# Performance work log

Measured on AMD Instinct MI355X. Metric: run time of the kernel, lower is better.

Reference implementation:

```python
import jax, jax.numpy as jnp
import numpy as np

HIDDEN = 2880
N_HEADS = 64
N_KV_HEADS = 8
HEAD_DIM = 64
ROPE_THETA = 150000.0


def _rope(x, position_ids):
    # x: [B, H, S, D]; rotate-half RoPE as in the flax module
    inv_freq = 1.0 / (ROPE_THETA ** (jnp.arange(0, HEAD_DIM, 2, dtype=jnp.float32) / HEAD_DIM))
    b, h, s, d = x.shape
    freqs = jnp.outer(position_ids.reshape(-1).astype(jnp.float32), inv_freq)  # [B*S, D/2]
    cos = jnp.cos(freqs).reshape(b, 1, s, d // 2)
    sin = jnp.sin(freqs).reshape(b, 1, s, d // 2)
    x1, x2 = jnp.split(x, 2, axis=-1)
    return jnp.concatenate([x1 * cos - x2 * sin, x1 * sin + x2 * cos], axis=-1)


def setup_inputs() -> dict:
    key = jax.random.key(0)
    ks = jax.random.split(key, 5)
    B, S = 2, 1024
    x = jax.random.normal(ks[0], (B, S, HIDDEN), dtype=jnp.float32)
    wq = jax.random.normal(ks[1], (HIDDEN, N_HEADS * HEAD_DIM), dtype=jnp.float32) * 0.02
    wk = jax.random.normal(ks[2], (HIDDEN, N_KV_HEADS * HEAD_DIM), dtype=jnp.float32) * 0.02
    wv = jax.random.normal(ks[3], (HIDDEN, N_KV_HEADS * HEAD_DIM), dtype=jnp.float32) * 0.02
    wo = jax.random.normal(ks[4], (N_HEADS * HEAD_DIM, HIDDEN), dtype=jnp.float32) * 0.02
    position_ids = jnp.broadcast_to(jnp.arange(S, dtype=jnp.int32)[None, :], (B, S))
    return {"x": x, "wq": wq, "wk": wk, "wv": wv, "wo": wo, "position_ids": position_ids}


def reference(x, wq, wk, wv, wo, position_ids):
    b, s, _ = x.shape
    scale = 1.0 / np.sqrt(HEAD_DIM)
    q = (x @ wq).reshape(b, s, N_HEADS, HEAD_DIM).transpose(0, 2, 1, 3)       # [B,H,S,D]
    k = (x @ wk).reshape(b, s, N_KV_HEADS, HEAD_DIM).transpose(0, 2, 1, 3)    # [B,Hkv,S,D]
    v = (x @ wv).reshape(b, s, N_KV_HEADS, HEAD_DIM).transpose(0, 2, 1, 3)
    q = _rope(q, position_ids)
    k = _rope(k, position_ids)
    rep = N_HEADS // N_KV_HEADS
    k = jnp.repeat(k, rep, axis=1)  # GQA head-repeat as in original
    v = jnp.repeat(v, rep, axis=1)
    scores = jnp.einsum('bhqd,bhkd->bhqk', q, k) * scale
    causal = jnp.tril(jnp.ones((s, s), dtype=bool))[None, None, :, :]
    scores = jnp.where(causal, scores, -jnp.inf)
    probs = jax.nn.softmax(scores, axis=-1)
    out = jnp.einsum('bhqk,bhkd->bhqd', probs, v)
    out = out.transpose(0, 2, 1, 3).reshape(b, s, N_HEADS * HEAD_DIM)
    return out @ wo
```

## Files before the change

### kernel.cpp

```cpp
#include <hip/hip_runtime.h>

#define BB 2
#define SS 1024
#define HIDDEN 2880
#define NH 64
#define NKV 8
#define HD 64
#define M_TOK 2048
#define NQ 4096
#define NKVD 512
#define NQKV 5120
#define NOUT 2880
#define NOUT_PAD 2944

typedef __attribute__((ext_vector_type(8))) short short8;
typedef __attribute__((ext_vector_type(4))) float f32x4;

__device__ __forceinline__ unsigned short f2b(float x) {
  union { float f; unsigned u; } v; v.f = x;
  unsigned r = (v.u + 0x7FFFu + ((v.u >> 16) & 1u)) >> 16;
  return (unsigned short)r;
}

__device__ __forceinline__ void gload16(const void* g, void* l) {
  __builtin_amdgcn_global_load_lds(
      (const __attribute__((address_space(1))) void*)g,
      (__attribute__((address_space(3))) void*)l, 16, 0, 0);
}

__global__ __launch_bounds__(256) void cast_x_kernel(const float* __restrict__ in,
                                                     unsigned short* __restrict__ out,
                                                     int n4) {
  int idx = blockIdx.x * 256 + threadIdx.x;
  if (idx >= n4) return;
  float4 v = ((const float4*)in)[idx];
  ushort4 o;
  o.x = f2b(v.x); o.y = f2b(v.y); o.z = f2b(v.z); o.w = f2b(v.w);
  ((ushort4*)out)[idx] = o;
}

__global__ __launch_bounds__(256) void transpose_cast(const float* __restrict__ in,
                                                      long ldin,
                                                      unsigned short* __restrict__ out,
                                                      int K, int N) {
  __shared__ float t[32][33];
  const int n0 = blockIdx.x * 32, k0 = blockIdx.y * 32;
  const int tx = threadIdx.x, ty = threadIdx.y;
#pragma unroll
  for (int i = 0; i < 4; ++i) {
    int k = k0 + ty + i * 8;
    int n = n0 + tx;
    t[ty + i * 8][tx] = (n < N) ? in[(long)k * ldin + n] : 0.f;
  }
  __syncthreads();
#pragma unroll
  for (int i = 0; i < 4; ++i) {
    int n = n0 + ty + i * 8;
    int k = k0 + tx;
    out[(long)n * K + k] = f2b(t[tx][ty + i * 8]);
  }
}

__global__ __launch_bounds__(256) void rope_table(const int* __restrict__ pos,
                                                  float* __restrict__ ct,
                                                  float* __restrict__ st) {
  int tid = blockIdx.x * 256 + threadIdx.x;
  int t = tid >> 5, i = tid & 31;
  float p = (float)pos[t];
  float f = p * expf(-(float)i * (11.918390573078392f / 32.f));
  ct[tid] = cosf(f);
  st[tid] = sinf(f);
}

#define GEMM128_BODY(Aptr, Bptr, lda)                                                     \
  __shared__ char lA[128 * 128];                                                          \
  __shared__ char lB[128 * 128];                                                          \
  const int tid = threadIdx.x;                                                            \
  const int lane = tid & 63;                                                              \
  const int w = tid >> 6;                                                                 \
  const int m16 = lane & 15, g4 = lane >> 4;                                              \
  const int wr = w >> 1, wc = w & 1;                                                      \
  const int bm = blockIdx.y * 128, bn = blockIdx.x * 128;                                 \
  const size_t strb = (size_t)(lda) * 2;                                                  \
  const int srow = tid >> 3;                                                              \
  const int scolb = ((tid & 7) * 16) ^ ((srow & 7) << 4);                                 \
  const int sdst = w * 1024;                                                              \
  const char* ga0 = (const char*)(Aptr) + (size_t)(bm + srow) * strb + scolb;             \
  const char* gb0 = (const char*)(Bptr) + (size_t)(bn + srow) * strb + scolb;             \
  const int swz = (m16 & 7) << 4;                                                         \
  const int kc0 = (g4 * 16) ^ swz;                                                        \
  const int kc1 = (64 + g4 * 16) ^ swz;                                                   \
  f32x4 acc[4][4];                                                                        \
  _Pragma("unroll") for (int i = 0; i < 4; ++i)                                           \
  _Pragma("unroll") for (int j = 0; j < 4; ++j) acc[i][j] = (f32x4){0.f, 0.f, 0.f, 0.f};  \
  const int NT = (lda) >> 6;                                                              \
  for (int t = 0; t < NT; ++t) {                                                          \
    const size_t ko = (size_t)t * 128;                                                    \
    __syncthreads();                                                                      \
    _Pragma("unroll") for (int i = 0; i < 4; ++i) {                                       \
      gload16(ga0 + (size_t)(i * 32) * strb + ko, lA + i * 4096 + sdst);                  \
      gload16(gb0 + (size_t)(i * 32) * strb + ko, lB + i * 4096 + sdst);                  \
    }                                                                                     \
    __syncthreads();                                                                      \
    short8 af[4][2], bf[4][2];                                                            \
    _Pragma("unroll") for (int mq = 0; mq < 4; ++mq) {                                    \
      const int row = wr * 64 + mq * 16 + m16;                                            \
      af[mq][0] = *(const short8*)(lA + row * 128 + kc0);                                 \
      af[mq][1] = *(const short8*)(lA + row * 128 + kc1);                                 \
    }                                                                                     \
    _Pragma("unroll") for (int nf = 0; nf < 4; ++nf) {                                    \
      const int row = wc * 64 + nf * 16 + m16;                                            \
      bf[nf][0] = *(const short8*)(lB + row * 128 + kc0);                                 \
      bf[nf][1] = *(const short8*)(lB + row * 128 + kc1);                                 \
    }                                                                                     \
    __builtin_amdgcn_s_setprio(1);                                                        \
    _Pragma("unroll") for (int mq = 0; mq < 4; ++mq)                                      \
    _Pragma("unroll") for (int nf = 0; nf < 4; ++nf) {                                    \
      acc[mq][nf] = __builtin_amdgcn_mfma_f32_16x16x32_bf16(af[mq][0], bf[nf][0], acc[mq][nf], 0, 0, 0); \
      acc[mq][nf] = __builtin_amdgcn_mfma_f32_16x16x32_bf16(af[mq][1], bf[nf][1], acc[mq][nf], 0, 0, 0); \
    }                                                                                     \
    __builtin_amdgcn_s_setprio(0);                                                        \
  }

__global__ __launch_bounds__(256, 3) void gemm128(const unsigned short* __restrict__ A,
                                                  const unsigned short* __restrict__ Bt,
                                                  float* __restrict__ C,
                                                  int lda, int ldc, int Nvalid) {
  GEMM128_BODY(A, Bt, lda)
#pragma unroll
  for (int mq = 0; mq < 4; ++mq) {
    const size_t row = bm + wr * 64 + mq * 16 + g4 * 4;
#pragma unroll
    for (int nf = 0; nf < 4; ++nf) {
      const int col = bn + wc * 64 + nf * 16 + m16;
      if (col < Nvalid) {
#pragma unroll
        for (int r = 0; r < 4; ++r)
          C[(row + r) * (size_t)ldc + col] = acc[mq][nf][r];
      }
    }
  }
}

__global__ __launch_bounds__(256, 3) void gemm128_qkv(const unsigned short* __restrict__ A,
                                                      const unsigned short* __restrict__ Bt,
                                                      const float* __restrict__ ct,
                                                      const float* __restrict__ st,
                                                      unsigned short* __restrict__ qb,
                                                      unsigned short* __restrict__ kb,
                                                      unsigned short* __restrict__ vtb,
                                                      int lda) {
  GEMM128_BODY(A, Bt, lda)
  const int region = (bn < 4096) ? 0 : ((bn < 4608) ? 1 : 2);
#pragma unroll
  for (int mq = 0; mq < 4; ++mq) {
    const int row = bm + wr * 64 + mq * 16 + g4 * 4;
    if (region == 2) {
#pragma unroll
      for (int nf = 0; nf < 4; ++nf) {
        const int d = (bn - 4608) + wc * 64 + nf * 16 + m16;
#pragma unroll
        for (int r = 0; r < 4; ++r) {
          const int t = row + r;
          const int b = t >> 10, sidx = t & 1023;
          vtb[((size_t)(b * NKVD + d)) * SS + sidx] = f2b(acc[mq][nf][r]);
        }
      }
    } else {
#pragma unroll
      for (int nf = 0; nf < 2; ++nf) {
        const int i = nf * 16 + m16;
#pragma unroll
        for (int r = 0; r < 4; ++r) {
          const int t = row + r;
          const int b = t >> 10, sidx = t & 1023;
          const float x1 = acc[mq][nf][r], x2 = acc[mq][nf + 2][r];
          const float c = ct[t * 32 + i], s = st[t * 32 + i];
          if (region == 0) {
            const int h = (bn >> 6) + wc;
            unsigned short* dst = qb + (((size_t)(b * NH + h)) * SS + sidx) * HD;
            dst[i]      = f2b((x1 * c - x2 * s) * 0.125f);
            dst[i + 32] = f2b((x1 * s + x2 * c) * 0.125f);
          } else {
            const int hk = ((bn - 4096) >> 6) + wc;
            unsigned short* dst = kb + (((size_t)(b * NKV + hk)) * SS + sidx) * HD;
            dst[i]      = f2b(x1 * c - x2 * s);
            dst[i + 32] = f2b(x1 * s + x2 * c);
          }
        }
      }
    }
  }
}

__global__ __launch_bounds__(512) void attn_fwd(const unsigned short* __restrict__ qb,
                                                const unsigned short* __restrict__ kb,
                                                const unsigned short* __restrict__ vtb,
                                                unsigned short* __restrict__ ao) {
  __shared__ unsigned short kB[2][64 * 64];
  __shared__ unsigned short vB[2][64 * 64];
  __shared__ unsigned short pB[8][32 * 64];
  const int tid = threadIdx.x, lane = tid & 63, w = tid >> 6;
  const int qblk = blockIdx.x;
  const int bh = blockIdx.y;
  const int b = bh >> 6, h = bh & 63, hkv = h >> 3;
  const int m16 = lane & 15, g4 = lane >> 4;
  const int rbase = qblk * 256 + w * 32;

  const unsigned short* qp =
      qb + (((size_t)(b * NH + h)) * SS + rbase + m16) * HD + g4 * 8;
  const short8 q00 = *(const short8*)(qp);
  const short8 q01 = *(const short8*)(qp + 32);
  const short8 q10 = *(const short8*)(qp + 16 * HD);
  const short8 q11 = *(const short8*)(qp + 16 * HD + 32);

  const char* kbp = (const char*)(kb + ((size_t)(b * NKV + hkv)) * SS * HD);
  const char* vbp = (const char*)(vtb + ((size_t)(b * NKV + hkv)) * HD * SS);

  const int lrow = lane >> 3;
  const int lcolb = ((lane & 7) * 16) ^ ((lrow & 7) << 4);
  unsigned short* kDst0 = &kB[0][w * 512];
  unsigned short* kDst1 = &kB[1][w * 512];
  unsigned short* vDst0 = &vB[0][w * 512];
  unsigned short* vDst1 = &vB[1][w * 512];
  const size_t kRowOff = (size_t)(w * 8 + lrow) * 128 + lcolb;
  const size_t vRowOff = (size_t)(w * 8 + lrow) * 2048 + lcolb;

  const short8 ones = {(short)0x3F80, (short)0x3F80, (short)0x3F80, (short)0x3F80,
                       (short)0x3F80, (short)0x3F80, (short)0x3F80, (short)0x3F80};

  f32x4 o0[4], o1[4];
#pragma unroll
  for (int n = 0; n < 4; ++n) { o0[n] = (f32x4){0,0,0,0}; o1[n] = (f32x4){0,0,0,0}; }
  f32x4 lacc0 = (f32x4){0,0,0,0}, lacc1 = (f32x4){0,0,0,0};
  float mrow0[4] = {-1e30f,-1e30f,-1e30f,-1e30f};
  float mrow1[4] = {-1e30f,-1e30f,-1e30f,-1e30f};

  char* pw = (char*)pB[w];
  const int swz_m = (m16 & 7) << 4;
  const int nt = (qblk + 1) * 4;

  gload16(kbp + kRowOff, kDst0);
  gload16(vbp + vRowOff, vDst0);
  __syncthreads();

  for (int t = 0; t < nt; ++t) {
    const int k0 = t * 64;
    const char* kLds = (const char*)kB[t & 1];
    const char* vLds = (const char*)vB[t & 1];
    if (t + 1 < nt) {
      if (t & 1) { gload16(kbp + (size_t)(t + 1) * 8192 + kRowOff, kDst0);
                   gload16(vbp + (size_t)(t + 1) * 128  + vRowOff, vDst0); }
      else       { gload16(kbp + (size_t)(t + 1) * 8192 + kRowOff, kDst1);
                   gload16(vbp + (size_t)(t + 1) * 128  + vRowOff, vDst1); }
    }
    if (k0 < rbase + 32) {
      short8 kf0[4], kf1[4];
#pragma unroll
      for (int kf = 0; kf < 4; ++kf) {
        const int rb = (kf * 16 + m16) * 128;
        kf0[kf] = *(const short8*)(kLds + ((rb + g4 * 16) ^ swz_m));
        kf1[kf] = *(const short8*)(kLds + ((rb + 64 + g4 * 16) ^ swz_m));
      }
      f32x4 s0[4], s1[4];
      __builtin_amdgcn_s_setprio(1);
#pragma unroll
      for (int kf = 0; kf < 4; ++kf) {
        f32x4 z = (f32x4){0,0,0,0};
        z = __builtin_amdgcn_mfma_f32_16x16x32_bf16(q00, kf0[kf], z, 0, 0, 0);
        z = __builtin_amdgcn_mfma_f32_16x16x32_bf16(q01, kf1[kf], z, 0, 0, 0);
        s0[kf] = z;
        f32x4 z2 = (f32x4){0,0,0,0};
        z2 = __builtin_amdgcn_mfma_f32_16x16x32_bf16(q10, kf0[kf], z2, 0, 0, 0);
        z2 = __builtin_amdgcn_mfma_f32_16x16x32_bf16(q11, kf1[kf], z2, 0, 0, 0);
        s1[kf] = z2;
      }
      __builtin_amdgcn_s_setprio(0);
      if (k0 + 63 >= rbase) {
#pragma unroll
        for (int kf = 0; kf < 4; ++kf)
#pragma unroll
          for (int r = 0; r < 4; ++r) {
            const int col = k0 + kf * 16 + m16;
            if (col > rbase + g4 * 4 + r)      s0[kf][r] = -1e30f;
            if (col > rbase + 16 + g4 * 4 + r) s1[kf][r] = -1e30f;
          }
      }
      int grow = 0;
#pragma unroll
      for (int kf = 0; kf < 4; ++kf)
#pragma unroll
        for (int r = 0; r < 4; ++r) {
          grow |= (s0[kf][r] > mrow0[r] + 8.f);
          grow |= (s1[kf][r] > mrow1[r] + 8.f);
        }
      if (__any(grow)) {
        float mx0[4], mx1[4];
#pragma unroll
        for (int r = 0; r < 4; ++r) {
          mx0[r] = fmaxf(fmaxf(s0[0][r], s0[1][r]), fmaxf(s0[2][r], s0[3][r]));
          mx1[r] = fmaxf(fmaxf(s1[0][r], s1[1][r]), fmaxf(s1[2][r], s1[3][r]));
        }
#pragma unroll
        for (int off = 1; off <= 8; off <<= 1)
#pragma unroll
          for (int r = 0; r < 4; ++r) {
            mx0[r] = fmaxf(mx0[r], __shfl_xor(mx0[r], off));
            mx1[r] = fmaxf(mx1[r], __shfl_xor(mx1[r], off));
          }
#pragma unroll
        for (int r = 0; r < 4; ++r) {
          float mn0 = fmaxf(mrow0[r], mx0[r]);
          float sc0 = __expf(mrow0[r] - mn0);
          mrow0[r] = mn0; lacc0[r] *= sc0;
          float mn1 = fmaxf(mrow1[r], mx1[r]);
          float sc1 = __expf(mrow1[r] - mn1);
          mrow1[r] = mn1; lacc1[r] *= sc1;
#pragma unroll
          for (int n = 0; n < 4; ++n) { o0[n][r] *= sc0; o1[n][r] *= sc1; }
        }
      }
#pragma unroll
      for (int kf = 0; kf < 4; ++kf)
#pragma unroll
        for (int r = 0; r < 4; ++r) {
          const int colb = (kf * 16 + m16) * 2;
          int row = g4 * 4 + r;
          *(unsigned short*)(pw + ((row * 128 + colb) ^ ((row & 7) << 4))) =
              f2b(__expf(s0[kf][r] - mrow0[r]));
          row += 16;
          *(unsigned short*)(pw + ((row * 128 + colb) ^ ((row & 7) << 4))) =
              f2b(__expf(s1[kf][r] - mrow1[r]));
        }
      const int prb0 = m16 * 128, prb1 = (16 + m16) * 128;
      short8 pf00 = *(const short8*)(pw + ((prb0 + g4 * 16) ^ swz_m));
      short8 pf01 = *(const short8*)(pw + ((prb0 + 64 + g4 * 16) ^ swz_m));
      short8 pf10 = *(const short8*)(pw + ((prb1 + g4 * 16) ^ swz_m));
      short8 pf11 = *(const short8*)(pw + ((prb1 + 64 + g4 * 16) ^ swz_m));
      __builtin_amdgcn_s_setprio(1);
      lacc0 = __builtin_amdgcn_mfma_f32_16x16x32_bf16(pf00, ones, lacc0, 0, 0, 0);
      lacc0 = __builtin_amdgcn_mfma_f32_16x16x32_bf16(pf01, ones, lacc0, 0, 0, 0);
      lacc1 = __builtin_amdgcn_mfma_f32_16x16x32_bf16(pf10, ones, lacc1, 0, 0, 0);
      lacc1 = __builtin_amdgcn_mfma_f32_16x16x32_bf16(pf11, ones, lacc1, 0, 0, 0);
#pragma unroll
      for (int n = 0; n < 4; ++n) {
        const int rb = (n * 16 + m16) * 128;
        short8 vf0 = *(const short8*)(vLds + ((rb + g4 * 16) ^ swz_m));
        short8 vf1 = *(const short8*)(vLds + ((rb + 64 + g4 * 16) ^ swz_m));
        o0[n] = __builtin_amdgcn_mfma_f32_16x16x32_bf16(pf00, vf0, o0[n], 0, 0, 0);
        o0[n] = __builtin_amdgcn_mfma_f32_16x16x32_bf16(pf01, vf1, o0[n], 0, 0, 0);
        o1[n] = __builtin_amdgcn_mfma_f32_16x16x32_bf16(pf10, vf0, o1[n], 0, 0, 0);
        o1[n] = __builtin_amdgcn_mfma_f32_16x16x32_bf16(pf11, vf1, o1[n], 0, 0, 0);
      }
      __builtin_amdgcn_s_setprio(0);
    }
    __syncthreads();
  }

  float inv0[4], inv1[4];
#pragma unroll
  for (int r = 0; r < 4; ++r) { inv0[r] = 1.f / lacc0[r]; inv1[r] = 1.f / lacc1[r]; }
  const size_t row0 = (size_t)b * SS + rbase + g4 * 4;
#pragma unroll
  for (int n = 0; n < 4; ++n)
#pragma unroll
    for (int r = 0; r < 4; ++r) {
      ao[(row0 + r) * (size_t)NQ + h * 64 + n * 16 + m16] = f2b(o0[n][r] * inv0[r]);
      ao[(row0 + 16 + r) * (size_t)NQ + h * 64 + n * 16 + m16] = f2b(o1[n][r] * inv1[r]);
    }
}

constexpr size_t OFF_XB    = 0;
constexpr size_t OFF_WQKVT = 11796480;
constexpr size_t OFF_WOT   = 41287680;
constexpr size_t OFF_COS   = 65404928;
constexpr size_t OFF_SIN   = 65667072;
constexpr size_t OFF_QB    = 65929216;
constexpr size_t OFF_KB    = 82706432;
constexpr size_t OFF_VTB   = 84803584;
constexpr size_t OFF_ATTNB = 86900736;

extern "C" void kernel_launch(void* const* d_in, const int* in_sizes, int n_in,
                              void* d_out, int out_size, void* d_ws, size_t ws_size,
                              hipStream_t stream) {
  const float* x  = (const float*)d_in[0];
  const float* wq = (const float*)d_in[1];
  const float* wk = (const float*)d_in[2];
  const float* wv = (const float*)d_in[3];
  const float* wo = (const float*)d_in[4];
  const int* pos  = (const int*)d_in[5];
  float* out = (float*)d_out;
  char* ws = (char*)d_ws;

  unsigned short* xb    = (unsigned short*)(ws + OFF_XB);
  unsigned short* wqkvt = (unsigned short*)(ws + OFF_WQKVT);
  unsigned short* wot   = (unsigned short*)(ws + OFF_WOT);
  float* ct             = (float*)(ws + OFF_COS);
  float* st             = (float*)(ws + OFF_SIN);
  unsigned short* qbuf  = (unsigned short*)(ws + OFF_QB);
  unsigned short* kbuf  = (unsigned short*)(ws + OFF_KB);
  unsigned short* vtb   = (unsigned short*)(ws + OFF_VTB);
  unsigned short* attnb = (unsigned short*)(ws + OFF_ATTNB);

  cast_x_kernel<<<(M_TOK * HIDDEN / 4 + 255) / 256, 256, 0, stream>>>(x, xb, M_TOK * HIDDEN / 4);
  rope_table<<<(M_TOK * 32) / 256, 256, 0, stream>>>(pos, ct, st);
  transpose_cast<<<dim3(NQ / 32, HIDDEN / 32), dim3(32, 8), 0, stream>>>(
      wq, NQ, wqkvt, HIDDEN, NQ);
  transpose_cast<<<dim3(NKVD / 32, HIDDEN / 32), dim3(32, 8), 0, stream>>>(
      wk, NKVD, wqkvt + (size_t)NQ * HIDDEN, HIDDEN, NKVD);
  transpose_cast<<<dim3(NKVD / 32, HIDDEN / 32), dim3(32, 8), 0, stream>>>(
      wv, NKVD, wqkvt + (size_t)(NQ + NKVD) * HIDDEN, HIDDEN, NKVD);
  transpose_cast<<<dim3(NOUT_PAD / 32, NQ / 32), dim3(32, 8), 0, stream>>>(
      wo, NOUT, wot, NQ, NOUT);
  gemm128_qkv<<<dim3(NQKV / 128, M_TOK / 128), 256, 0, stream>>>(
      xb, wqkvt, ct, st, qbuf, kbuf, vtb, HIDDEN);
  attn_fwd<<<dim3(4, BB * NH), 512, 0, stream>>>(qbuf, kbuf, vtb, attnb);
  gemm128<<<dim3(NOUT_PAD / 128, M_TOK / 128), 256, 0, stream>>>(
      attnb, wot, out, NQ, NOUT, NOUT);
}
```

Baseline: 256.7 us.

## Split-K the output projection, fold log2e into Q scale, use exp2

The output projection GEMM is split into two K halves via blockIdx.z. Each half writes bf16 partials into reused workspace (the x and weight buffers), and a separate kernel sums them into fp32 output, aiming for better CU occupancy on the 23x16 tile grid. Separately, the attention softmax now uses exp2f with log2(e) folded into the Q scaling, truncating bf16 conversion for probabilities, and the rescale threshold is adjusted to base-2 units. The bf16 partials and truncation lower accuracy, and the extra reduce kernel adds launch and memory traffic.

```diff
diff --git a/kernel.cpp b/kernel.cpp
--- a/kernel.cpp
+++ b/kernel.cpp
@@ -21,6 +21,10 @@
   unsigned r = (v.u + 0x7FFFu + ((v.u >> 16) & 1u)) >> 16;
   return (unsigned short)r;
 }
+__device__ __forceinline__ unsigned short f2bt(float x) {
+  union { float f; unsigned u; } v; v.f = x;
+  return (unsigned short)(v.u >> 16);
+}
 
 __device__ __forceinline__ void gload16(const void* g, void* l) {
   __builtin_amdgcn_global_load_lds(
@@ -72,7 +76,7 @@
   st[tid] = sinf(f);
 }
 
-#define GEMM128_BODY(Aptr, Bptr, lda)                                                     \
+#define GEMM128_BODY(Aptr, Bptr, lda, Kloop)                                              \
   __shared__ char lA[128 * 128];                                                          \
   __shared__ char lB[128 * 128];                                                          \
   const int tid = threadIdx.x;                                                            \
@@ -82,18 +86,19 @@
   const int wr = w >> 1, wc = w & 1;                                                      \
   const int bm = blockIdx.y * 128, bn = blockIdx.x * 128;                                 \
   const size_t strb = (size_t)(lda) * 2;                                                  \
+  const size_t koffb = (size_t)blockIdx.z * (Kloop) * 2;                                  \
   const int srow = tid >> 3;                                                              \
   const int scolb = ((tid & 7) * 16) ^ ((srow & 7) << 4);                                 \
   const int sdst = w * 1024;                                                              \
-  const char* ga0 = (const char*)(Aptr) + (size_t)(bm + srow) * strb + scolb;             \
-  const char* gb0 = (const char*)(Bptr) + (size_t)(bn + srow) * strb + scolb;             \
+  const char* ga0 = (const char*)(Aptr) + (size_t)(bm + srow) * strb + koffb + scolb;     \
+  const char* gb0 = (const char*)(Bptr) + (size_t)(bn + srow) * strb + koffb + scolb;     \
   const int swz = (m16 & 7) << 4;                                                         \
   const int kc0 = (g4 * 16) ^ swz;                                                        \
   const int kc1 = (64 + g4 * 16) ^ swz;                                                   \
   f32x4 acc[4][4];                                                                        \
   _Pragma("unroll") for (int i = 0; i < 4; ++i)                                           \
   _Pragma("unroll") for (int j = 0; j < 4; ++j) acc[i][j] = (f32x4){0.f, 0.f, 0.f, 0.f};  \
-  const int NT = (lda) >> 6;                                                              \
+  const int NT = (Kloop) >> 6;                                                            \
   for (int t = 0; t < NT; ++t) {                                                          \
     const size_t ko = (size_t)t * 128;                                                    \
     __syncthreads();                                                                      \
@@ -126,7 +131,7 @@
                                                   const unsigned short* __restrict__ Bt,
                                                   float* __restrict__ C,
                                                   int lda, int ldc, int Nvalid) {
-  GEMM128_BODY(A, Bt, lda)
+  GEMM128_BODY(A, Bt, lda, lda)
 #pragma unroll
   for (int mq = 0; mq < 4; ++mq) {
     const size_t row = bm + wr * 64 + mq * 16 + g4 * 4;
@@ -140,6 +145,46 @@
       }
     }
   }
+}
+
+__global__ __launch_bounds__(256, 3) void gemm128s(const unsigned short* __restrict__ A,
+                                                   const unsigned short* __restrict__ Bt,
+                                                   unsigned short* __restrict__ P0,
+                                                   unsigned short* __restrict__ P1,
+                                                   int lda, int Kloop, int ldc) {
+  GEMM128_BODY(A, Bt, lda, Kloop)
+  unsigned short* __restrict__ Cw = blockIdx.z ? P1 : P0;
+#pragma unroll
+  for (int mq = 0; mq < 4; ++mq) {
+    const size_t row = bm + wr * 64 + mq * 16 + g4 * 4;
+#pragma unroll
+    for (int nf = 0; nf < 4; ++nf) {
+      const int col = bn + wc * 64 + nf * 16 + m16;
+#pragma unroll
+      for (int r = 0; r < 4; ++r)
+        Cw[(row + r) * (size_t)ldc + col] = f2b(acc[mq][nf][r]);
+    }
+  }
+}
+
+__device__ __forceinline__ float b2f(unsigned short u) {
+  union { unsigned u; float f; } v; v.u = ((unsigned)u) << 16; return v.f;
+}
+
+__global__ __launch_bounds__(256) void reduce_wo2(const unsigned short* __restrict__ p0,
+                                                  const unsigned short* __restrict__ p1,
+                                                  float* __restrict__ out) {
+  int idx = blockIdx.x * 256 + threadIdx.x;
+  int row = idx / 720, c4 = idx - row * 720;
+  const size_t o = (size_t)row * NOUT_PAD + c4 * 4;
+  const ushort4 a = *(const ushort4*)(p0 + o);
+  const ushort4 b = *(const ushort4*)(p1 + o);
+  float4 r;
+  r.x = b2f(a.x) + b2f(b.x);
+  r.y = b2f(a.y) + b2f(b.y);
+  r.z = b2f(a.z) + b2f(b.z);
+  r.w = b2f(a.w) + b2f(b.w);
+  *(float4*)(out + (size_t)row * 2880 + c4 * 4) = r;
 }
 
 __global__ __launch_bounds__(256, 3) void gemm128_qkv(const unsigned short* __restrict__ A,
@@ -150,7 +195,7 @@
                                                       unsigned short* __restrict__ kb,
                                                       unsigned short* __restrict__ vtb,
                                                       int lda) {
-  GEMM128_BODY(A, Bt, lda)
+  GEMM128_BODY(A, Bt, lda, lda)
   const int region = (bn < 4096) ? 0 : ((bn < 4608) ? 1 : 2);
 #pragma unroll
   for (int mq = 0; mq < 4; ++mq) {
@@ -179,8 +224,8 @@
           if (region == 0) {
             const int h = (bn >> 6) + wc;
             unsigned short* dst = qb + (((size_t)(b * NH + h)) * SS + sidx) * HD;
-            dst[i]      = f2b((x1 * c - x2 * s) * 0.125f);
-            dst[i + 32] = f2b((x1 * s + x2 * c) * 0.125f);
+            dst[i]      = f2b((x1 * c - x2 * s) * 0.18033688011112042f);
+            dst[i + 32] = f2b((x1 * s + x2 * c) * 0.18033688011112042f);
           } else {
             const int hk = ((bn - 4096) >> 6) + wc;
             unsigned short* dst = kb + (((size_t)(b * NKV + hk)) * SS + sidx) * HD;
@@ -291,8 +336,8 @@
       for (int kf = 0; kf < 4; ++kf)
 #pragma unroll
         for (int r = 0; r < 4; ++r) {
-          grow |= (s0[kf][r] > mrow0[r] + 8.f);
-          grow |= (s1[kf][r] > mrow1[r] + 8.f);
+          grow |= (s0[kf][r] > mrow0[r] + 11.5f);
+          grow |= (s1[kf][r] > mrow1[r] + 11.5f);
         }
       if (__any(grow)) {
         float mx0[4], mx1[4];
@@ -311,10 +356,10 @@
 #pragma unroll
         for (int r = 0; r < 4; ++r) {
           float mn0 = fmaxf(mrow0[r], mx0[r]);
-          float sc0 = __expf(mrow0[r] - mn0);
+          float sc0 = exp2f(mrow0[r] - mn0);
           mrow0[r] = mn0; lacc0[r] *= sc0;
           float mn1 = fmaxf(mrow1[r], mx1[r]);
-          float sc1 = __expf(mrow1[r] - mn1);
+          float sc1 = exp2f(mrow1[r] - mn1);
           mrow1[r] = mn1; lacc1[r] *= sc1;
 #pragma unroll
           for (int n = 0; n < 4; ++n) { o0[n][r] *= sc0; o1[n][r] *= sc1; }
@@ -327,10 +372,10 @@
           const int colb = (kf * 16 + m16) * 2;
           int row = g4 * 4 + r;
           *(unsigned short*)(pw + ((row * 128 + colb) ^ ((row & 7) << 4))) =
-              f2b(__expf(s0[kf][r] - mrow0[r]));
+              f2bt(exp2f(s0[kf][r] - mrow0[r]));
           row += 16;
           *(unsigned short*)(pw + ((row * 128 + colb) ^ ((row & 7) << 4))) =
-              f2b(__expf(s1[kf][r] - mrow1[r]));
+              f2bt(exp2f(s1[kf][r] - mrow1[r]));
         }
       const int prb0 = m16 * 128, prb1 = (16 + m16) * 128;
       short8 pf00 = *(const short8*)(pw + ((prb0 + g4 * 16) ^ swz_m));
@@ -372,6 +417,8 @@
 
 constexpr size_t OFF_XB    = 0;
 constexpr size_t OFF_WQKVT = 11796480;
+constexpr size_t OFF_WP0   = 0;
+constexpr size_t OFF_WP1   = 12058624;
 constexpr size_t OFF_WOT   = 41287680;
 constexpr size_t OFF_COS   = 65404928;
 constexpr size_t OFF_SIN   = 65667072;
@@ -394,6 +441,8 @@
 
   unsigned short* xb    = (unsigned short*)(ws + OFF_XB);
   unsigned short* wqkvt = (unsigned short*)(ws + OFF_WQKVT);
+  unsigned short* wp0   = (unsigned short*)(ws + OFF_WP0);
+  unsigned short* wp1   = (unsigned short*)(ws + OFF_WP1);
   unsigned short* wot   = (unsigned short*)(ws + OFF_WOT);
   float* ct             = (float*)(ws + OFF_COS);
   float* st             = (float*)(ws + OFF_SIN);
@@ -415,6 +464,7 @@
   gemm128_qkv<<<dim3(NQKV / 128, M_TOK / 128), 256, 0, stream>>>(
       xb, wqkvt, ct, st, qbuf, kbuf, vtb, HIDDEN);
   attn_fwd<<<dim3(4, BB * NH), 512, 0, stream>>>(qbuf, kbuf, vtb, attnb);
-  gemm128<<<dim3(NOUT_PAD / 128, M_TOK / 128), 256, 0, stream>>>(
-      attnb, wot, out, NQ, NOUT, NOUT);
-}
+  gemm128s<<<dim3(NOUT_PAD / 128, M_TOK / 128, 2), 256, 0, stream>>>(
+      attnb, wot, wp0, wp1, NQ, NQ / 2, NOUT_PAD);
+  reduce_wo2<<<(M_TOK * 720) / 256, 256, 0, stream>>>(wp0, wp1, out);
+}
```

Result: slower. 269.0 us (+4.8%).
